# Optimization experiments

Hardware: AMD Instinct MI355X
Metric: run time of the kernel (lower is better)

Reference implementation:

```python
import jax, jax.numpy as jnp
import numpy as np

H = 64    # n_hidden
N = 1535  # input nodes; total graph nodes Nn = N + 1
B = 32    # batch
BN_EPS = 1e-5


def _p(key, shape, scale=0.05):
    return (jax.random.normal(key, shape, dtype=jnp.float32) * scale)


def setup_inputs() -> dict:
    key = jax.random.key(0)
    ks = jax.random.split(key, 32)
    inp = {
        'input_xx': jax.random.normal(ks[0], (B, N, 8), dtype=jnp.float32),
        'input_yy': jax.random.normal(ks[1], (B, N), dtype=jnp.float32),
        'output_xx': jax.random.normal(ks[2], (B, 1, 8), dtype=jnp.float32),
        # fc1: Linear(9, H); fc2: Linear(H, H)
        'W1': _p(ks[3], (H, 9)), 'b1': _p(ks[4], (H,)),
        'W2': _p(ks[5], (H, H)), 'b2': _p(ks[6], (H,)),
        # enc_new_x: Linear(8, H)
        'Wenc': _p(ks[7], (H, 8)), 'benc': _p(ks[8], (H,)),
        # Q, K, V: Linear(H, H)
        'WQ': _p(ks[9], (H, H)), 'bQ': _p(ks[10], (H,)),
        'WK': _p(ks[11], (H, H)), 'bK': _p(ks[12], (H,)),
        'WV': _p(ks[13], (H, H)), 'bV': _p(ks[14], (H,)),
        # QK: Linear(2H, 1) split into the q-half and k-half of its weight row
        'wQKq': _p(ks[15], (H,)), 'wQKk': _p(ks[16], (H,)),
        'bQK': _p(ks[17], ()),
        # A2N: Linear(H, H)
        'WA': _p(ks[18], (H, H)), 'bA': _p(ks[19], (H,)),
        # BatchNorm1d affine params
        'gamma': jnp.ones((H,), jnp.float32), 'beta': jnp.zeros((H,), jnp.float32),
        # heads
        'Wmu': _p(ks[20], (1, H)), 'bmu': _p(ks[21], (1,)),
        'Wsig': _p(ks[22], (1, H)), 'bsig': _p(ks[23], (1,)),
    }
    return inp


def _forward(input_xx, input_yy, output_xx, W1, b1, W2, b2, Wenc, benc,
             WQ, bQ, WK, bK, WV, bV, wQKq, wQKk, bQK, WA, bA,
             gamma, beta, Wmu, bmu, Wsig, bsig):
    # encode input nodes: cat(x, y) -> fc1 -> relu -> fc2 -> relu
    x = jnp.concatenate([input_xx, input_yy[..., None]], axis=-1)  # [B,N,9]
    h = jax.nn.relu(x @ W1.T + b1)
    h = jax.nn.relu(h @ W2.T + b2)                                  # [B,N,H]
    out_enc = jax.nn.relu(output_xx[:, 0, :] @ Wenc.T + benc)       # [B,H]
    # nodes: [Nn, B, H]  (node axis first, matching the torch list of nodes)
    nodes = jnp.concatenate([jnp.transpose(h, (1, 0, 2)), out_enc[None]], axis=0)

    def communicate(nodes):
        q = nodes @ WQ.T + bQ  # [Nn,B,H]
        k = nodes @ WK.T + bK
        v = nodes @ WV.T + bV
        # QK(cat(q,k)) decomposes additively: score[i,b,j] = q[i,b].wq + k[j,b].wk + b
        sq = q @ wQKq          # [Nn,B]
        sk = k @ wQKk          # [Nn,B]
        scores = sq[:, :, None] + sk.T[None, :, :] + bQK  # [Nn,B,Nn]
        w_att = jax.nn.softmax(scores, axis=-1)
        aggre = jnp.einsum('ibj,jbh->ibh', w_att, v)      # [Nn,B,H]
        z = aggre @ WA.T + bA
        # BatchNorm1d in training mode, applied per node over the batch axis
        mu = jnp.mean(z, axis=1, keepdims=True)
        var = jnp.var(z, axis=1, keepdims=True)
        z = (z - mu) / jnp.sqrt(var + BN_EPS) * gamma + beta
        return jax.nn.relu(z)

    for _ in range(4):
        nodes = communicate(nodes)

    agg = jnp.max(nodes, axis=0)                # [B,H]
    mu_out = agg @ Wmu.T + bmu                  # [B,1]
    sig_out = (agg @ Wsig.T + bsig) ** 2 + 0.01 # [B,1]
    return mu_out, sig_out


def reference(input_xx, input_yy, output_xx, W1, b1, W2, b2, Wenc, benc,
              WQ, bQ, WK, bK, WV, bV, wQKq, wQKk, bQK, WA, bA,
              gamma, beta, Wmu, bmu, Wsig, bsig):
    return _forward(input_xx, input_yy, output_xx, W1, b1, W2, b2, Wenc, benc,
                    WQ, bQ, WK, bK, WV, bV, wQKq, wQKk, bQK, WA, bA,
                    gamma, beta, Wmu, bmu, Wsig, bsig)
```

## Files before the change

kernel.cpp:

```cpp
#include <hip/hip_runtime.h>
#include <math.h>

#define HD    64
#define NIN   1535
#define NN    1536
#define BB    32
#define BN_EPS 1e-5f
#define CH    64
#define NCH   24

#define WS_M  0
#define WS_S  768
#define WS_V  1536

__global__ __launch_bounds__(256) void k_main(
    const float* __restrict__ xx,
    const float* __restrict__ yy,
    const float* __restrict__ oxx,
    const float* __restrict__ W1, const float* __restrict__ b1,
    const float* __restrict__ W2, const float* __restrict__ b2,
    const float* __restrict__ Wenc, const float* __restrict__ benc,
    const float* __restrict__ WK, const float* __restrict__ wQKk,
    float* __restrict__ ws) {
  __shared__ float W1s[576];
  __shared__ float b1s[64], b2s[64], bencs[64], us[64];
  __shared__ float Wencs[512];
  __shared__ float W2Ts[64 * 65];
  __shared__ float xs[512];
  __shared__ float ys[64];
  __shared__ float h1s[4][64];
  __shared__ float h2s[64 * 64];
  __shared__ float sks[64], e_s[64], rbuf[256], red0[1];

  const int t = threadIdx.x;
  const int blk = blockIdx.x;
  const int b = blk & 31;
  const int c = blk >> 5;
  const int pp = b * NCH + c;

  for (int e = t; e < 576; e += 256) W1s[e] = W1[e];
  for (int e = t; e < 512; e += 256) Wencs[e] = Wenc[e];
  for (int e = t; e < 4096; e += 256) {
    int h = e >> 6, k = e & 63;
    W2Ts[k * 65 + h] = W2[e];
  }
  for (int e = t; e < 512; e += 256) {
    int j = e >> 3, k = e & 7;
    int r0 = c * CH + j;
    xs[e] = (r0 < NIN) ? xx[(size_t)b * (NIN * 8) + (size_t)r0 * 8 + k]
                       : oxx[b * 8 + k];
  }
  if (t < 64) {
    b1s[t] = b1[t]; b2s[t] = b2[t]; bencs[t] = benc[t];
    int r0 = c * CH + t;
    ys[t] = (r0 < NIN) ? yy[b * NIN + r0] : 0.f;
    float a = 0.f;
    #pragma unroll
    for (int h0 = 0; h0 < 64; h0++) a += wQKk[h0] * WK[h0 * 64 + t];
    us[t] = a;
  }
  __syncthreads();

  const int w = t >> 6, lane = t & 63;
  float* h1w = h1s[w];

  float w2r[64];
  #pragma unroll
  for (int k = 0; k < 64; k++) w2r[k] = W2Ts[k * 65 + lane];

  for (int rr = 0; rr < 16; rr++) {
    int j = w * 16 + rr;
    int r0 = c * CH + j;
    const float* xr = xs + j * 8;
    float h2;
    if (r0 < NIN) {
      const float* wr = W1s + lane * 9;
      float a = b1s[lane];
      a += xr[0] * wr[0] + xr[1] * wr[1] + xr[2] * wr[2] + xr[3] * wr[3];
      a += xr[4] * wr[4] + xr[5] * wr[5] + xr[6] * wr[6] + xr[7] * wr[7];
      a += ys[j] * wr[8];
      h1w[lane] = fmaxf(a, 0.f);
      float a0 = b2s[lane], a1 = 0.f;
      #pragma unroll
      for (int k = 0; k < 64; k += 4) {
        float4 hv = *(const float4*)(h1w + k);
        a0 += hv.x * w2r[k]     + hv.z * w2r[k + 2];
        a1 += hv.y * w2r[k + 1] + hv.w * w2r[k + 3];
      }
      h2 = fmaxf(a0 + a1, 0.f);
    } else {
      const float* wr = Wencs + lane * 8;
      float a = bencs[lane];
      #pragma unroll
      for (int k = 0; k < 8; k++) a += xr[k] * wr[k];
      h2 = fmaxf(a, 0.f);
    }
    h2s[j * 64 + lane] = h2;
    float p = h2 * us[lane];
    p += __shfl_down(p, 32); p += __shfl_down(p, 16); p += __shfl_down(p, 8);
    p += __shfl_down(p, 4);  p += __shfl_down(p, 2);  p += __shfl_down(p, 1);
    if (lane == 0) sks[j] = p;
  }
  __syncthreads();

  if (t < 64) {
    float m = sks[t];
    m = fmaxf(m, __shfl_down(m, 32)); m = fmaxf(m, __shfl_down(m, 16));
    m = fmaxf(m, __shfl_down(m, 8));  m = fmaxf(m, __shfl_down(m, 4));
    m = fmaxf(m, __shfl_down(m, 2));  m = fmaxf(m, __shfl_down(m, 1));
    if (t == 0) red0[0] = m;
  }
  __syncthreads();
  float M = red0[0];
  if (t < 64) {
    float e = expf(sks[t] - M);
    e_s[t] = e;
    float s = e;
    s += __shfl_down(s, 32); s += __shfl_down(s, 16); s += __shfl_down(s, 8);
    s += __shfl_down(s, 4);  s += __shfl_down(s, 2);  s += __shfl_down(s, 1);
    if (t == 0) { ws[WS_M + pp] = M; ws[WS_S + pp] = s; }
  }
  __syncthreads();
  {
    float acc = 0.f;
    for (int j = w; j < 64; j += 4) acc += e_s[j] * h2s[j * 64 + lane];
    rbuf[t] = acc;
    __syncthreads();
    if (t < 64)
      ws[WS_V + pp * 64 + t] =
          rbuf[t] + rbuf[64 + t] + rbuf[128 + t] + rbuf[192 + t];
  }
}

__global__ __launch_bounds__(256) void k_tail(
    const float* __restrict__ ws,
    const float* __restrict__ WV, const float* __restrict__ bV,
    const float* __restrict__ WA, const float* __restrict__ bA,
    const float* __restrict__ gamma, const float* __restrict__ beta,
    const float* __restrict__ Wmu, const float* __restrict__ bmu,
    const float* __restrict__ Wsig, const float* __restrict__ bsig,
    float* __restrict__ out) {
  __shared__ float WAs[64 * 65];
  __shared__ float WVs[4096];
  __shared__ float WAVT[4096];
  __shared__ float bAVs[64];
  __shared__ float Ml[768], Sl[768], wexp[768];
  __shared__ float Mb[32], iSb[32];
  __shared__ float st[32 * 66];
  __shared__ float zs[32 * 66];
  __shared__ float scs[64], shs[64];
  const int t = threadIdx.x;

  for (int e = t; e < 4096; e += 256) {
    int h = e >> 6, m = e & 63;
    WAs[h * 65 + m] = WA[e];
    WVs[e] = WV[e];
  }
  for (int p = t; p < 768; p += 256) {
    Ml[p] = ws[WS_M + p];
    Sl[p] = ws[WS_S + p];
  }
  __syncthreads();

  if (t < 64) {
    float a = bA[t];
    #pragma unroll
    for (int k = 0; k < 64; k++) a += WAs[t * 65 + k] * bV[k];
    bAVs[t] = a;
  }
  {
    int kg = t >> 6, h = t & 63;
    float acc[16];
    #pragma unroll
    for (int kk = 0; kk < 16; kk++) acc[kk] = 0.f;
    for (int m = 0; m < 64; m++) {
      float wa = WAs[h * 65 + m];
      const float4* wv = (const float4*)(WVs + m * 64 + kg * 16);
      float4 w0 = wv[0], w1 = wv[1], w2 = wv[2], w3 = wv[3];
      acc[0]  += wa * w0.x; acc[1]  += wa * w0.y; acc[2]  += wa * w0.z; acc[3]  += wa * w0.w;
      acc[4]  += wa * w1.x; acc[5]  += wa * w1.y; acc[6]  += wa * w1.z; acc[7]  += wa * w1.w;
      acc[8]  += wa * w2.x; acc[9]  += wa * w2.y; acc[10] += wa * w2.z; acc[11] += wa * w2.w;
      acc[12] += wa * w3.x; acc[13] += wa * w3.y; acc[14] += wa * w3.z; acc[15] += wa * w3.w;
    }
    #pragma unroll
    for (int kk = 0; kk < 16; kk++) WAVT[(kg * 16 + kk) * 64 + h] = acc[kk];
  }
  if (t < 32) {
    float m = -1e30f;
    for (int cc = 0; cc < NCH; cc++) m = fmaxf(m, Ml[t * NCH + cc]);
    Mb[t] = m;
  }
  __syncthreads();
  for (int p = t; p < 768; p += 256) {
    int bb = p / NCH;
    wexp[p] = expf(Ml[p] - Mb[bb]);
  }
  __syncthreads();
  if (t < 32) {
    float s = 0.f;
    for (int cc = 0; cc < NCH; cc++) {
      int p = t * NCH + cc;
      s += Sl[p] * wexp[p];
    }
    iSb[t] = 1.0f / s;
  }
  __syncthreads();
  {
    int bb = t >> 3, hg = t & 7;
    float acc[8];
    #pragma unroll
    for (int jj = 0; jj < 8; jj++) acc[jj] = 0.f;
    for (int cc = 0; cc < NCH; cc++) {
      int p = bb * NCH + cc;
      float wgt = wexp[p];
      const float* vp = ws + WS_V + p * 64 + hg;
      #pragma unroll
      for (int jj = 0; jj < 8; jj++) acc[jj] += wgt * vp[jj * 8];
    }
    float is = iSb[bb];
    #pragma unroll
    for (int jj = 0; jj < 8; jj++) st[bb * 66 + hg + 8 * jj] = acc[jj] * is;
  }
  __syncthreads();

  for (int r = 0; r < 4; r++) {
    {
      int bb = t >> 3, hg = t & 7;
      float acc[8];
      #pragma unroll
      for (int jj = 0; jj < 8; jj++) acc[jj] = bAVs[hg + 8 * jj];
      for (int k = 0; k < 64; k++) {
        float v = st[bb * 66 + k];
        const float* wp = WAVT + k * 64 + hg;
        #pragma unroll
        for (int jj = 0; jj < 8; jj++) acc[jj] += v * wp[8 * jj];
      }
      #pragma unroll
      for (int jj = 0; jj < 8; jj++) zs[bb * 66 + hg + 8 * jj] = acc[jj];
    }
    __syncthreads();
    if (t < 64) {
      float s1 = 0.f;
      for (int bb2 = 0; bb2 < BB; bb2++) s1 += zs[bb2 * 66 + t];
      float mu = s1 * (1.0f / BB);
      float s2 = 0.f;
      for (int bb2 = 0; bb2 < BB; bb2++) {
        float d = zs[bb2 * 66 + t] - mu;
        s2 += d * d;
      }
      float inv = gamma[t] / sqrtf(s2 * (1.0f / BB) + BN_EPS);
      scs[t] = inv;
      shs[t] = beta[t] - mu * inv;
    }
    __syncthreads();
    for (int e = t; e < BB * 64; e += 256) {
      int bb2 = e >> 6, hh = e & 63;
      st[bb2 * 66 + hh] = fmaxf(zs[bb2 * 66 + hh] * scs[hh] + shs[hh], 0.f);
    }
    __syncthreads();
  }

  if (t < BB) {
    const float* nr = st + t * 66;
    float m = bmu[0], sg = bsig[0];
    #pragma unroll 8
    for (int h = 0; h < 64; h++) {
      float v = nr[h];
      m += v * Wmu[h];
      sg += v * Wsig[h];
    }
    out[t] = m;
    out[BB + t] = sg * sg + 0.01f;
  }
}

extern "C" void kernel_launch(void* const* d_in, const int* in_sizes, int n_in,
                              void* d_out, int out_size, void* d_ws, size_t ws_size,
                              hipStream_t stream) {
  const float* xx   = (const float*)d_in[0];
  const float* yy   = (const float*)d_in[1];
  const float* oxx  = (const float*)d_in[2];
  const float* W1   = (const float*)d_in[3];
  const float* b1   = (const float*)d_in[4];
  const float* W2   = (const float*)d_in[5];
  const float* b2   = (const float*)d_in[6];
  const float* Wenc = (const float*)d_in[7];
  const float* benc = (const float*)d_in[8];
  const float* WK   = (const float*)d_in[11];
  const float* WV   = (const float*)d_in[13];
  const float* bV   = (const float*)d_in[14];
  const float* wQKk = (const float*)d_in[16];
  const float* WA   = (const float*)d_in[18];
  const float* bA   = (const float*)d_in[19];
  const float* gamma= (const float*)d_in[20];
  const float* beta = (const float*)d_in[21];
  const float* Wmu  = (const float*)d_in[22];
  const float* bmu  = (const float*)d_in[23];
  const float* Wsig = (const float*)d_in[24];
  const float* bsig = (const float*)d_in[25];

  float* ws  = (float*)d_ws;
  float* out = (float*)d_out;

  k_main<<<BB * NCH, 256, 0, stream>>>(xx, yy, oxx, W1, b1, W2, b2, Wenc, benc,
                                       WK, wQKk, ws);
  k_tail<<<1, 256, 0, stream>>>(ws, WV, bV, WA, bA, gamma, beta,
                                Wmu, bmu, Wsig, bsig, out);
}
```

Baseline: 148.2 us.

## Fuse main and tail kernels via last-block-done atomic counter

Merges the per-chunk encoder kernel and the single-block tail kernel into one launch, where the last block to finish (found with an atomic counter plus thread fences) runs the cross-chunk softmax merge, the folded WA·WV projection, the four BatchNorm rounds and the heads. Shared memory is unioned into one buffer, and WV is read straight from global memory instead of being staged. This removes one kernel launch and the gap between launches. In exchange it adds a memset launch for the counter, and the serial tail now runs inside a 768-block grid after the last block arrives.

```diff
diff --git a/kernel.cpp b/kernel.cpp
--- a/kernel.cpp
+++ b/kernel.cpp
@@ -8,269 +8,297 @@
 #define BN_EPS 1e-5f
 #define CH    64
 #define NCH   24
-
-#define WS_M  0
-#define WS_S  768
-#define WS_V  1536
-
-__global__ __launch_bounds__(256) void k_main(
-    const float* __restrict__ xx,
-    const float* __restrict__ yy,
+#define NBLK  (BB * NCH)
+
+#define WS_M   0
+#define WS_S   768
+#define WS_V   1536
+#define WS_CNT 50688
+#define CNT_BYTE_OFF (WS_CNT * 4)
+
+#define SM_W1  0
+#define SM_B1  576
+#define SM_B2  640
+#define SM_BE  704
+#define SM_U   768
+#define SM_WE  832
+#define SM_W2T 1344
+#define SM_X   5504
+#define SM_Y   6016
+#define SM_H1  6080
+#define SM_H2  6336
+#define SM_SK  10432
+#define SM_E   10496
+#define SM_RB  10560
+#define SM_R0  10816
+#define ST_WAVT 0
+#define ST_BAV  4096
+#define ST_ML   4160
+#define ST_SL   4928
+#define ST_WX   5696
+#define ST_MB   6464
+#define ST_ISB  6496
+#define ST_WA   6528
+#define ST_ST   6528
+#define ST_ZS   8640
+#define ST_SC   10752
+#define ST_SH   10816
+#define SMEM_F  10880
+
+__global__ __launch_bounds__(256) void k_fused(
+    const float* __restrict__ xx, const float* __restrict__ yy,
     const float* __restrict__ oxx,
     const float* __restrict__ W1, const float* __restrict__ b1,
     const float* __restrict__ W2, const float* __restrict__ b2,
     const float* __restrict__ Wenc, const float* __restrict__ benc,
     const float* __restrict__ WK, const float* __restrict__ wQKk,
-    float* __restrict__ ws) {
-  __shared__ float W1s[576];
-  __shared__ float b1s[64], b2s[64], bencs[64], us[64];
-  __shared__ float Wencs[512];
-  __shared__ float W2Ts[64 * 65];
-  __shared__ float xs[512];
-  __shared__ float ys[64];
-  __shared__ float h1s[4][64];
-  __shared__ float h2s[64 * 64];
-  __shared__ float sks[64], e_s[64], rbuf[256], red0[1];
-
+    const float* __restrict__ WV, const float* __restrict__ bV,
+    const float* __restrict__ WA, const float* __restrict__ bA,
+    const float* __restrict__ gamma, const float* __restrict__ beta,
+    const float* __restrict__ Wmu, const float* __restrict__ bmu,
+    const float* __restrict__ Wsig, const float* __restrict__ bsig,
+    float* __restrict__ ws, unsigned int* __restrict__ cnt,
+    float* __restrict__ out) {
+  __shared__ float S[SMEM_F];
   const int t = threadIdx.x;
   const int blk = blockIdx.x;
   const int b = blk & 31;
   const int c = blk >> 5;
   const int pp = b * NCH + c;
 
-  for (int e = t; e < 576; e += 256) W1s[e] = W1[e];
-  for (int e = t; e < 512; e += 256) Wencs[e] = Wenc[e];
-  for (int e = t; e < 4096; e += 256) {
-    int h = e >> 6, k = e & 63;
-    W2Ts[k * 65 + h] = W2[e];
+  {
+    float* W1s = S + SM_W1;  float* b1s = S + SM_B1;  float* b2s = S + SM_B2;
+    float* bencs = S + SM_BE; float* us = S + SM_U;   float* Wencs = S + SM_WE;
+    float* W2Ts = S + SM_W2T; float* xs = S + SM_X;   float* ys = S + SM_Y;
+    float* h2s = S + SM_H2;   float* sks = S + SM_SK; float* e_s = S + SM_E;
+    float* rbuf = S + SM_RB;  float* red0 = S + SM_R0;
+
+    for (int e = t; e < 576; e += 256) W1s[e] = W1[e];
+    for (int e = t; e < 512; e += 256) Wencs[e] = Wenc[e];
+    for (int e = t; e < 4096; e += 256) {
+      int h = e >> 6, k = e & 63;
+      W2Ts[k * 65 + h] = W2[e];
+    }
+    for (int e = t; e < 512; e += 256) {
+      int j = e >> 3, k = e & 7;
+      int r0 = c * CH + j;
+      xs[e] = (r0 < NIN) ? xx[(size_t)b * (NIN * 8) + (size_t)r0 * 8 + k]
+                         : oxx[b * 8 + k];
+    }
+    if (t < 64) {
+      b1s[t] = b1[t]; b2s[t] = b2[t]; bencs[t] = benc[t];
+      int r0 = c * CH + t;
+      ys[t] = (r0 < NIN) ? yy[b * NIN + r0] : 0.f;
+      float a = 0.f;
+      #pragma unroll
+      for (int h0 = 0; h0 < 64; h0++) a += wQKk[h0] * WK[h0 * 64 + t];
+      us[t] = a;
+    }
+    __syncthreads();
+
+    const int w = t >> 6, lane = t & 63;
+    float* h1w = S + SM_H1 + w * 64;
+
+    float w2r[64];
+    #pragma unroll
+    for (int k = 0; k < 64; k++) w2r[k] = W2Ts[k * 65 + lane];
+
+    for (int rr = 0; rr < 16; rr++) {
+      int j = w * 16 + rr;
+      int r0 = c * CH + j;
+      const float* xr = xs + j * 8;
+      float h2;
+      if (r0 < NIN) {
+        const float* wr = W1s + lane * 9;
+        float a = b1s[lane];
+        a += xr[0] * wr[0] + xr[1] * wr[1] + xr[2] * wr[2] + xr[3] * wr[3];
+        a += xr[4] * wr[4] + xr[5] * wr[5] + xr[6] * wr[6] + xr[7] * wr[7];
+        a += ys[j] * wr[8];
+        h1w[lane] = fmaxf(a, 0.f);
+        float a0 = b2s[lane], a1 = 0.f;
+        #pragma unroll
+        for (int k = 0; k < 64; k += 4) {
+          float4 hv = *(const float4*)(h1w + k);
+          a0 += hv.x * w2r[k]     + hv.z * w2r[k + 2];
+          a1 += hv.y * w2r[k + 1] + hv.w * w2r[k + 3];
+        }
+        h2 = fmaxf(a0 + a1, 0.f);
+      } else {
+        const float* wr = Wencs + lane * 8;
+        float a = bencs[lane];
+        #pragma unroll
+        for (int k = 0; k < 8; k++) a += xr[k] * wr[k];
+        h2 = fmaxf(a, 0.f);
+      }
+      h2s[j * 64 + lane] = h2;
+      float p = h2 * us[lane];
+      p += __shfl_down(p, 32); p += __shfl_down(p, 16); p += __shfl_down(p, 8);
+      p += __shfl_down(p, 4);  p += __shfl_down(p, 2);  p += __shfl_down(p, 1);
+      if (lane == 0) sks[j] = p;
+    }
+    __syncthreads();
+
+    if (t < 64) {
+      float m = sks[t];
+      m = fmaxf(m, __shfl_down(m, 32)); m = fmaxf(m, __shfl_down(m, 16));
+      m = fmaxf(m, __shfl_down(m, 8));  m = fmaxf(m, __shfl_down(m, 4));
+      m = fmaxf(m, __shfl_down(m, 2));  m = fmaxf(m, __shfl_down(m, 1));
+      if (t == 0) red0[0] = m;
+    }
+    __syncthreads();
+    float M = red0[0];
+    if (t < 64) {
+      float e = expf(sks[t] - M);
+      e_s[t] = e;
+      float s = e;
+      s += __shfl_down(s, 32); s += __shfl_down(s, 16); s += __shfl_down(s, 8);
+      s += __shfl_down(s, 4);  s += __shfl_down(s, 2);  s += __shfl_down(s, 1);
+      if (t == 0) { ws[WS_M + pp] = M; ws[WS_S + pp] = s; }
+    }
+    __syncthreads();
+    {
+      float acc = 0.f;
+      for (int j = w; j < 64; j += 4) acc += e_s[j] * h2s[j * 64 + lane];
+      rbuf[t] = acc;
+      __syncthreads();
+      if (t < 64)
+        ws[WS_V + pp * 64 + t] =
+            rbuf[t] + rbuf[64 + t] + rbuf[128 + t] + rbuf[192 + t];
+    }
   }
-  for (int e = t; e < 512; e += 256) {
-    int j = e >> 3, k = e & 7;
-    int r0 = c * CH + j;
-    xs[e] = (r0 < NIN) ? xx[(size_t)b * (NIN * 8) + (size_t)r0 * 8 + k]
-                       : oxx[b * 8 + k];
-  }
-  if (t < 64) {
-    b1s[t] = b1[t]; b2s[t] = b2[t]; bencs[t] = benc[t];
-    int r0 = c * CH + t;
-    ys[t] = (r0 < NIN) ? yy[b * NIN + r0] : 0.f;
-    float a = 0.f;
-    #pragma unroll
-    for (int h0 = 0; h0 < 64; h0++) a += wQKk[h0] * WK[h0 * 64 + t];
-    us[t] = a;
-  }
+
+  __threadfence();
   __syncthreads();
-
-  const int w = t >> 6, lane = t & 63;
-  float* h1w = h1s[w];
-
-  float w2r[64];
-  #pragma unroll
-  for (int k = 0; k < 64; k++) w2r[k] = W2Ts[k * 65 + lane];
-
-  for (int rr = 0; rr < 16; rr++) {
-    int j = w * 16 + rr;
-    int r0 = c * CH + j;
-    const float* xr = xs + j * 8;
-    float h2;
-    if (r0 < NIN) {
-      const float* wr = W1s + lane * 9;
-      float a = b1s[lane];
-      a += xr[0] * wr[0] + xr[1] * wr[1] + xr[2] * wr[2] + xr[3] * wr[3];
-      a += xr[4] * wr[4] + xr[5] * wr[5] + xr[6] * wr[6] + xr[7] * wr[7];
-      a += ys[j] * wr[8];
-      h1w[lane] = fmaxf(a, 0.f);
-      float a0 = b2s[lane], a1 = 0.f;
-      #pragma unroll
-      for (int k = 0; k < 64; k += 4) {
-        float4 hv = *(const float4*)(h1w + k);
-        a0 += hv.x * w2r[k]     + hv.z * w2r[k + 2];
-        a1 += hv.y * w2r[k + 1] + hv.w * w2r[k + 3];
-      }
-      h2 = fmaxf(a0 + a1, 0.f);
-    } else {
-      const float* wr = Wencs + lane * 8;
-      float a = bencs[lane];
-      #pragma unroll
-      for (int k = 0; k < 8; k++) a += xr[k] * wr[k];
-      h2 = fmaxf(a, 0.f);
-    }
-    h2s[j * 64 + lane] = h2;
-    float p = h2 * us[lane];
-    p += __shfl_down(p, 32); p += __shfl_down(p, 16); p += __shfl_down(p, 8);
-    p += __shfl_down(p, 4);  p += __shfl_down(p, 2);  p += __shfl_down(p, 1);
-    if (lane == 0) sks[j] = p;
-  }
+  if (t == 0) S[SM_R0] = (float)(atomicAdd(cnt, 1u) == NBLK - 1 ? 1 : 0);
   __syncthreads();
-
-  if (t < 64) {
-    float m = sks[t];
-    m = fmaxf(m, __shfl_down(m, 32)); m = fmaxf(m, __shfl_down(m, 16));
-    m = fmaxf(m, __shfl_down(m, 8));  m = fmaxf(m, __shfl_down(m, 4));
-    m = fmaxf(m, __shfl_down(m, 2));  m = fmaxf(m, __shfl_down(m, 1));
-    if (t == 0) red0[0] = m;
-  }
+  if (S[SM_R0] == 0.f) return;
+  __threadfence();
   __syncthreads();
-  float M = red0[0];
-  if (t < 64) {
-    float e = expf(sks[t] - M);
-    e_s[t] = e;
-    float s = e;
-    s += __shfl_down(s, 32); s += __shfl_down(s, 16); s += __shfl_down(s, 8);
-    s += __shfl_down(s, 4);  s += __shfl_down(s, 2);  s += __shfl_down(s, 1);
-    if (t == 0) { ws[WS_M + pp] = M; ws[WS_S + pp] = s; }
-  }
-  __syncthreads();
+
   {
-    float acc = 0.f;
-    for (int j = w; j < 64; j += 4) acc += e_s[j] * h2s[j * 64 + lane];
-    rbuf[t] = acc;
-    __syncthreads();
-    if (t < 64)
-      ws[WS_V + pp * 64 + t] =
-          rbuf[t] + rbuf[64 + t] + rbuf[128 + t] + rbuf[192 + t];
-  }
-}
-
-__global__ __launch_bounds__(256) void k_tail(
-    const float* __restrict__ ws,
-    const float* __restrict__ WV, const float* __restrict__ bV,
-    const float* __restrict__ WA, const float* __restrict__ bA,
-    const float* __restrict__ gamma, const float* __restrict__ beta,
-    const float* __restrict__ Wmu, const float* __restrict__ bmu,
-    const float* __restrict__ Wsig, const float* __restrict__ bsig,
-    float* __restrict__ out) {
-  __shared__ float WAs[64 * 65];
-  __shared__ float WVs[4096];
-  __shared__ float WAVT[4096];
-  __shared__ float bAVs[64];
-  __shared__ float Ml[768], Sl[768], wexp[768];
-  __shared__ float Mb[32], iSb[32];
-  __shared__ float st[32 * 66];
-  __shared__ float zs[32 * 66];
-  __shared__ float scs[64], shs[64];
-  const int t = threadIdx.x;
-
-  for (int e = t; e < 4096; e += 256) {
-    int h = e >> 6, m = e & 63;
-    WAs[h * 65 + m] = WA[e];
-    WVs[e] = WV[e];
-  }
-  for (int p = t; p < 768; p += 256) {
-    Ml[p] = ws[WS_M + p];
-    Sl[p] = ws[WS_S + p];
-  }
-  __syncthreads();
-
-  if (t < 64) {
-    float a = bA[t];
-    #pragma unroll
-    for (int k = 0; k < 64; k++) a += WAs[t * 65 + k] * bV[k];
-    bAVs[t] = a;
-  }
-  {
-    int kg = t >> 6, h = t & 63;
-    float acc[16];
-    #pragma unroll
-    for (int kk = 0; kk < 16; kk++) acc[kk] = 0.f;
-    for (int m = 0; m < 64; m++) {
-      float wa = WAs[h * 65 + m];
-      const float4* wv = (const float4*)(WVs + m * 64 + kg * 16);
-      float4 w0 = wv[0], w1 = wv[1], w2 = wv[2], w3 = wv[3];
-      acc[0]  += wa * w0.x; acc[1]  += wa * w0.y; acc[2]  += wa * w0.z; acc[3]  += wa * w0.w;
-      acc[4]  += wa * w1.x; acc[5]  += wa * w1.y; acc[6]  += wa * w1.z; acc[7]  += wa * w1.w;
-      acc[8]  += wa * w2.x; acc[9]  += wa * w2.y; acc[10] += wa * w2.z; acc[11] += wa * w2.w;
-      acc[12] += wa * w3.x; acc[13] += wa * w3.y; acc[14] += wa * w3.z; acc[15] += wa * w3.w;
-    }
-    #pragma unroll
-    for (int kk = 0; kk < 16; kk++) WAVT[(kg * 16 + kk) * 64 + h] = acc[kk];
-  }
-  if (t < 32) {
-    float m = -1e30f;
-    for (int cc = 0; cc < NCH; cc++) m = fmaxf(m, Ml[t * NCH + cc]);
-    Mb[t] = m;
-  }
-  __syncthreads();
-  for (int p = t; p < 768; p += 256) {
-    int bb = p / NCH;
-    wexp[p] = expf(Ml[p] - Mb[bb]);
-  }
-  __syncthreads();
-  if (t < 32) {
-    float s = 0.f;
-    for (int cc = 0; cc < NCH; cc++) {
-      int p = t * NCH + cc;
-      s += Sl[p] * wexp[p];
-    }
-    iSb[t] = 1.0f / s;
-  }
-  __syncthreads();
-  {
-    int bb = t >> 3, hg = t & 7;
-    float acc[8];
-    #pragma unroll
-    for (int jj = 0; jj < 8; jj++) acc[jj] = 0.f;
-    for (int cc = 0; cc < NCH; cc++) {
-      int p = bb * NCH + cc;
-      float wgt = wexp[p];
-      const float* vp = ws + WS_V + p * 64 + hg;
-      #pragma unroll
-      for (int jj = 0; jj < 8; jj++) acc[jj] += wgt * vp[jj * 8];
-    }
-    float is = iSb[bb];
-    #pragma unroll
-    for (int jj = 0; jj < 8; jj++) st[bb * 66 + hg + 8 * jj] = acc[jj] * is;
-  }
-  __syncthreads();
-
-  for (int r = 0; r < 4; r++) {
+    float* WAVT = S + ST_WAVT; float* bAVs = S + ST_BAV;
+    float* Ml = S + ST_ML;  float* Sl = S + ST_SL;  float* wexp = S + ST_WX;
+    float* Mb = S + ST_MB;  float* iSb = S + ST_ISB;
+    float* WAs = S + ST_WA; float* st = S + ST_ST;  float* zs = S + ST_ZS;
+    float* scs = S + ST_SC; float* shs = S + ST_SH;
+
+    for (int e = t; e < 4096; e += 256) {
+      int h = e >> 6, m = e & 63;
+      WAs[h * 65 + m] = WA[e];
+    }
+    for (int p = t; p < 768; p += 256) {
+      Ml[p] = ws[WS_M + p];
+      Sl[p] = ws[WS_S + p];
+    }
+    __syncthreads();
+
+    if (t < 64) {
+      float a = bA[t];
+      #pragma unroll
+      for (int k = 0; k < 64; k++) a += WAs[t * 65 + k] * bV[k];
+      bAVs[t] = a;
+    }
+    if (t < 32) {
+      float m = -1e30f;
+      for (int cc = 0; cc < NCH; cc++) m = fmaxf(m, Ml[t * NCH + cc]);
+      Mb[t] = m;
+    }
+    {
+      int kg = t >> 6, h = t & 63;
+      float acc[16];
+      #pragma unroll
+      for (int kk = 0; kk < 16; kk++) acc[kk] = 0.f;
+      for (int m = 0; m < 64; m++) {
+        float wa = WAs[h * 65 + m];
+        const float4* wv = (const float4*)(WV + m * 64 + kg * 16);
+        float4 w0 = wv[0], w1 = wv[1], w2 = wv[2], w3 = wv[3];
+        acc[0]  += wa * w0.x; acc[1]  += wa * w0.y; acc[2]  += wa * w0.z; acc[3]  += wa * w0.w;
+        acc[4]  += wa * w1.x; acc[5]  += wa * w1.y; acc[6]  += wa * w1.z; acc[7]  += wa * w1.w;
+        acc[8]  += wa * w2.x; acc[9]  += wa * w2.y; acc[10] += wa * w2.z; acc[11] += wa * w2.w;
+        acc[12] += wa * w3.x; acc[13] += wa * w3.y; acc[14] += wa * w3.z; acc[15] += wa * w3.w;
+      }
+      #pragma unroll
+      for (int kk = 0; kk < 16; kk++) WAVT[(kg * 16 + kk) * 64 + h] = acc[kk];
+    }
+    __syncthreads();
+    for (int p = t; p < 768; p += 256) wexp[p] = expf(Ml[p] - Mb[p / NCH]);
+    __syncthreads();
+    if (t < 32) {
+      float s = 0.f;
+      for (int cc = 0; cc < NCH; cc++) {
+        int p = t * NCH + cc;
+        s += Sl[p] * wexp[p];
+      }
+      iSb[t] = 1.0f / s;
+    }
+    __syncthreads();
     {
       int bb = t >> 3, hg = t & 7;
       float acc[8];
       #pragma unroll
-      for (int jj = 0; jj < 8; jj++) acc[jj] = bAVs[hg + 8 * jj];
-      for (int k = 0; k < 64; k++) {
-        float v = st[bb * 66 + k];
-        const float* wp = WAVT + k * 64 + hg;
-        #pragma unroll
-        for (int jj = 0; jj < 8; jj++) acc[jj] += v * wp[8 * jj];
-      }
-      #pragma unroll
-      for (int jj = 0; jj < 8; jj++) zs[bb * 66 + hg + 8 * jj] = acc[jj];
-    }
-    __syncthreads();
-    if (t < 64) {
-      float s1 = 0.f;
-      for (int bb2 = 0; bb2 < BB; bb2++) s1 += zs[bb2 * 66 + t];
-      float mu = s1 * (1.0f / BB);
-      float s2 = 0.f;
-      for (int bb2 = 0; bb2 < BB; bb2++) {
-        float d = zs[bb2 * 66 + t] - mu;
-        s2 += d * d;
-      }
-      float inv = gamma[t] / sqrtf(s2 * (1.0f / BB) + BN_EPS);
-      scs[t] = inv;
-      shs[t] = beta[t] - mu * inv;
-    }
-    __syncthreads();
-    for (int e = t; e < BB * 64; e += 256) {
-      int bb2 = e >> 6, hh = e & 63;
-      st[bb2 * 66 + hh] = fmaxf(zs[bb2 * 66 + hh] * scs[hh] + shs[hh], 0.f);
-    }
-    __syncthreads();
-  }
-
-  if (t < BB) {
-    const float* nr = st + t * 66;
-    float m = bmu[0], sg = bsig[0];
-    #pragma unroll 8
-    for (int h = 0; h < 64; h++) {
-      float v = nr[h];
-      m += v * Wmu[h];
-      sg += v * Wsig[h];
-    }
-    out[t] = m;
-    out[BB + t] = sg * sg + 0.01f;
+      for (int jj = 0; jj < 8; jj++) acc[jj] = 0.f;
+      for (int cc = 0; cc < NCH; cc++) {
+        int p = bb * NCH + cc;
+        float wgt = wexp[p];
+        const float* vp = ws + WS_V + p * 64 + hg;
+        #pragma unroll
+        for (int jj = 0; jj < 8; jj++) acc[jj] += wgt * vp[jj * 8];
+      }
+      float is = iSb[bb];
+      #pragma unroll
+      for (int jj = 0; jj < 8; jj++) st[bb * 66 + hg + 8 * jj] = acc[jj] * is;
+    }
+    __syncthreads();
+
+    for (int r = 0; r < 4; r++) {
+      {
+        int bb = t >> 3, hg = t & 7;
+        float acc[8];
+        #pragma unroll
+        for (int jj = 0; jj < 8; jj++) acc[jj] = bAVs[hg + 8 * jj];
+        for (int k = 0; k < 64; k++) {
+          float v = st[bb * 66 + k];
+          const float* wp = WAVT + k * 64 + hg;
+          #pragma unroll
+          for (int jj = 0; jj < 8; jj++) acc[jj] += v * wp[8 * jj];
+        }
+        #pragma unroll
+        for (int jj = 0; jj < 8; jj++) zs[bb * 66 + hg + 8 * jj] = acc[jj];
+      }
+      __syncthreads();
+      if (t < 64) {
+        float s1 = 0.f;
+        for (int bb2 = 0; bb2 < BB; bb2++) s1 += zs[bb2 * 66 + t];
+        float mu = s1 * (1.0f / BB);
+        float s2 = 0.f;
+        for (int bb2 = 0; bb2 < BB; bb2++) {
+          float d = zs[bb2 * 66 + t] - mu;
+          s2 += d * d;
+        }
+        float inv = gamma[t] / sqrtf(s2 * (1.0f / BB) + BN_EPS);
+        scs[t] = inv;
+        shs[t] = beta[t] - mu * inv;
+      }
+      __syncthreads();
+      for (int e = t; e < BB * 64; e += 256) {
+        int bb2 = e >> 6, hh = e & 63;
+        st[bb2 * 66 + hh] = fmaxf(zs[bb2 * 66 + hh] * scs[hh] + shs[hh], 0.f);
+      }
+      __syncthreads();
+    }
+
+    if (t < BB) {
+      const float* nr = st + t * 66;
+      float m = bmu[0], sg = bsig[0];
+      #pragma unroll 8
+      for (int h = 0; h < 64; h++) {
+        float v = nr[h];
+        m += v * Wmu[h];
+        sg += v * Wsig[h];
+      }
+      out[t] = m;
+      out[BB + t] = sg * sg + 0.01f;
+    }
   }
 }
 
@@ -299,11 +327,12 @@
   const float* Wsig = (const float*)d_in[24];
   const float* bsig = (const float*)d_in[25];
 
-  float* ws  = (float*)d_ws;
+  float* ws = (float*)d_ws;
+  unsigned int* cnt = (unsigned int*)((char*)d_ws + CNT_BYTE_OFF);
   float* out = (float*)d_out;
 
-  k_main<<<BB * NCH, 256, 0, stream>>>(xx, yy, oxx, W1, b1, W2, b2, Wenc, benc,
-                                       WK, wQKk, ws);
-  k_tail<<<1, 256, 0, stream>>>(ws, WV, bV, WA, bA, gamma, beta,
-                                Wmu, bmu, Wsig, bsig, out);
+  hipMemsetAsync(cnt, 0, 4, stream);
+  k_fused<<<NBLK, 256, 0, stream>>>(xx, yy, oxx, W1, b1, W2, b2, Wenc, benc,
+                                    WK, wQKk, WV, bV, WA, bA, gamma, beta,
+                                    Wmu, bmu, Wsig, bsig, ws, cnt, out);
 }
```

Measured after the change: 206.9 us. 39.6% more time.

## Move WA·WV precompute into extra main-kernel block and use online softmax per wave

Applied to the files above, without the earlier changes.

Adds one extra block to the main grid that computes the WA·WV product and fused bias into workspace, so the single-block tail kernel no longer does that serial matmul. The main kernel drops the shared-memory weight staging and instead loads W1/W2 rows straight into registers. It broadcasts h1 across lanes with readlane rather than through LDS. An online softmax per wave replaces the stored h2 tile and its multi-pass reductions. This cuts shared memory and barriers, at the cost of more global weight reads per block and faster-but-less-precise __expf.

```diff
diff --git a/kernel.cpp b/kernel.cpp
--- a/kernel.cpp
+++ b/kernel.cpp
@@ -1,57 +1,79 @@
 #include <hip/hip_runtime.h>
 #include <math.h>
 
-#define HD    64
 #define NIN   1535
 #define NN    1536
 #define BB    32
 #define BN_EPS 1e-5f
 #define CH    64
 #define NCH   24
-
-#define WS_M  0
-#define WS_S  768
-#define WS_V  1536
+#define NBLK  (BB * NCH)
+
+#define WS_M    0
+#define WS_S    768
+#define WS_V    1536
+#define WS_WAVT 50688
+#define WS_BAV  54784
+
+__device__ __forceinline__ float rdlane(float v, int l) {
+  return __int_as_float(__builtin_amdgcn_readlane(__float_as_int(v), l));
+}
 
 __global__ __launch_bounds__(256) void k_main(
-    const float* __restrict__ xx,
-    const float* __restrict__ yy,
+    const float* __restrict__ xx, const float* __restrict__ yy,
     const float* __restrict__ oxx,
     const float* __restrict__ W1, const float* __restrict__ b1,
     const float* __restrict__ W2, const float* __restrict__ b2,
     const float* __restrict__ Wenc, const float* __restrict__ benc,
     const float* __restrict__ WK, const float* __restrict__ wQKk,
+    const float* __restrict__ WV, const float* __restrict__ bV,
+    const float* __restrict__ WA, const float* __restrict__ bA,
     float* __restrict__ ws) {
-  __shared__ float W1s[576];
-  __shared__ float b1s[64], b2s[64], bencs[64], us[64];
-  __shared__ float Wencs[512];
-  __shared__ float W2Ts[64 * 65];
   __shared__ float xs[512];
   __shared__ float ys[64];
-  __shared__ float h1s[4][64];
-  __shared__ float h2s[64 * 64];
-  __shared__ float sks[64], e_s[64], rbuf[256], red0[1];
+  __shared__ float us[64];
+  __shared__ float cm[4], cs[4];
+  __shared__ float cvec[4][64];
 
   const int t = threadIdx.x;
   const int blk = blockIdx.x;
+
+  if (blk == NBLK) {
+    int kg = t >> 6, h = t & 63;
+    float acc[16];
+    #pragma unroll
+    for (int kk = 0; kk < 16; kk++) acc[kk] = 0.f;
+    for (int m = 0; m < 64; m++) {
+      float wa = WA[h * 64 + m];
+      const float4* wv = (const float4*)(WV + m * 64 + kg * 16);
+      float4 w0 = wv[0], w1 = wv[1], w2 = wv[2], w3 = wv[3];
+      acc[0]  += wa * w0.x; acc[1]  += wa * w0.y; acc[2]  += wa * w0.z; acc[3]  += wa * w0.w;
+      acc[4]  += wa * w1.x; acc[5]  += wa * w1.y; acc[6]  += wa * w1.z; acc[7]  += wa * w1.w;
+      acc[8]  += wa * w2.x; acc[9]  += wa * w2.y; acc[10] += wa * w2.z; acc[11] += wa * w2.w;
+      acc[12] += wa * w3.x; acc[13] += wa * w3.y; acc[14] += wa * w3.z; acc[15] += wa * w3.w;
+    }
+    #pragma unroll
+    for (int kk = 0; kk < 16; kk++)
+      ws[WS_WAVT + (kg * 16 + kk) * 64 + h] = acc[kk];
+    if (t < 64) {
+      float a = bA[t];
+      #pragma unroll
+      for (int k = 0; k < 64; k++) a += WA[t * 64 + k] * bV[k];
+      ws[WS_BAV + t] = a;
+    }
+    return;
+  }
+
   const int b = blk & 31;
   const int c = blk >> 5;
   const int pp = b * NCH + c;
 
-  for (int e = t; e < 576; e += 256) W1s[e] = W1[e];
-  for (int e = t; e < 512; e += 256) Wencs[e] = Wenc[e];
-  for (int e = t; e < 4096; e += 256) {
-    int h = e >> 6, k = e & 63;
-    W2Ts[k * 65 + h] = W2[e];
-  }
   for (int e = t; e < 512; e += 256) {
     int j = e >> 3, k = e & 7;
     int r0 = c * CH + j;
-    xs[e] = (r0 < NIN) ? xx[(size_t)b * (NIN * 8) + (size_t)r0 * 8 + k]
-                       : oxx[b * 8 + k];
+    xs[e] = (r0 < NIN) ? xx[((size_t)b * NIN + r0) * 8 + k] : oxx[b * 8 + k];
   }
   if (t < 64) {
-    b1s[t] = b1[t]; b2s[t] = b2[t]; bencs[t] = benc[t];
     int r0 = c * CH + t;
     ys[t] = (r0 < NIN) ? yy[b * NIN + r0] : 0.f;
     float a = 0.f;
@@ -62,86 +84,85 @@
   __syncthreads();
 
   const int w = t >> 6, lane = t & 63;
-  float* h1w = h1s[w];
 
   float w2r[64];
+  {
+    const float4* wr = (const float4*)(W2 + lane * 64);
+    #pragma unroll
+    for (int q = 0; q < 16; q++) {
+      float4 v = wr[q];
+      w2r[4 * q] = v.x; w2r[4 * q + 1] = v.y;
+      w2r[4 * q + 2] = v.z; w2r[4 * q + 3] = v.w;
+    }
+  }
+  float w1r[9];
   #pragma unroll
-  for (int k = 0; k < 64; k++) w2r[k] = W2Ts[k * 65 + lane];
-
+  for (int i = 0; i < 9; i++) w1r[i] = W1[lane * 9 + i];
+  const float b1v = b1[lane], b2v = b2[lane], uv = us[lane];
+
+  float m_run = -1e30f, s_run = 0.f, acc_v = 0.f;
   for (int rr = 0; rr < 16; rr++) {
     int j = w * 16 + rr;
     int r0 = c * CH + j;
-    const float* xr = xs + j * 8;
+    float4 x0 = *(const float4*)(xs + j * 8);
+    float4 x1 = *(const float4*)(xs + j * 8 + 4);
     float h2;
     if (r0 < NIN) {
-      const float* wr = W1s + lane * 9;
-      float a = b1s[lane];
-      a += xr[0] * wr[0] + xr[1] * wr[1] + xr[2] * wr[2] + xr[3] * wr[3];
-      a += xr[4] * wr[4] + xr[5] * wr[5] + xr[6] * wr[6] + xr[7] * wr[7];
-      a += ys[j] * wr[8];
-      h1w[lane] = fmaxf(a, 0.f);
-      float a0 = b2s[lane], a1 = 0.f;
+      float a = b1v;
+      a += x0.x * w1r[0] + x0.y * w1r[1] + x0.z * w1r[2] + x0.w * w1r[3];
+      a += x1.x * w1r[4] + x1.y * w1r[5] + x1.z * w1r[6] + x1.w * w1r[7];
+      a += ys[j] * w1r[8];
+      float h1v = fmaxf(a, 0.f);
+      float a0 = b2v, a1 = 0.f, a2 = 0.f, a3 = 0.f;
       #pragma unroll
       for (int k = 0; k < 64; k += 4) {
-        float4 hv = *(const float4*)(h1w + k);
-        a0 += hv.x * w2r[k]     + hv.z * w2r[k + 2];
-        a1 += hv.y * w2r[k + 1] + hv.w * w2r[k + 3];
+        a0 += rdlane(h1v, k)     * w2r[k];
+        a1 += rdlane(h1v, k + 1) * w2r[k + 1];
+        a2 += rdlane(h1v, k + 2) * w2r[k + 2];
+        a3 += rdlane(h1v, k + 3) * w2r[k + 3];
       }
-      h2 = fmaxf(a0 + a1, 0.f);
+      h2 = fmaxf((a0 + a1) + (a2 + a3), 0.f);
     } else {
-      const float* wr = Wencs + lane * 8;
-      float a = bencs[lane];
-      #pragma unroll
-      for (int k = 0; k < 8; k++) a += xr[k] * wr[k];
+      const float4* we = (const float4*)(Wenc + lane * 8);
+      float4 w0 = we[0], w1v = we[1];
+      float a = benc[lane];
+      a += x0.x * w0.x + x0.y * w0.y + x0.z * w0.z + x0.w * w0.w;
+      a += x1.x * w1v.x + x1.y * w1v.y + x1.z * w1v.z + x1.w * w1v.w;
       h2 = fmaxf(a, 0.f);
     }
-    h2s[j * 64 + lane] = h2;
-    float p = h2 * us[lane];
-    p += __shfl_down(p, 32); p += __shfl_down(p, 16); p += __shfl_down(p, 8);
-    p += __shfl_down(p, 4);  p += __shfl_down(p, 2);  p += __shfl_down(p, 1);
-    if (lane == 0) sks[j] = p;
-  }
-  __syncthreads();
-
+    float p = h2 * uv;
+    p += __shfl_xor(p, 1);  p += __shfl_xor(p, 2);  p += __shfl_xor(p, 4);
+    p += __shfl_xor(p, 8);  p += __shfl_xor(p, 16); p += __shfl_xor(p, 32);
+    float mn = fmaxf(m_run, p);
+    float f  = __expf(m_run - mn);
+    float e  = __expf(p - mn);
+    s_run = s_run * f + e;
+    acc_v = acc_v * f + e * h2;
+    m_run = mn;
+  }
+
+  if (lane == 0) { cm[w] = m_run; cs[w] = s_run; }
+  cvec[w][lane] = acc_v;
+  __syncthreads();
   if (t < 64) {
-    float m = sks[t];
-    m = fmaxf(m, __shfl_down(m, 32)); m = fmaxf(m, __shfl_down(m, 16));
-    m = fmaxf(m, __shfl_down(m, 8));  m = fmaxf(m, __shfl_down(m, 4));
-    m = fmaxf(m, __shfl_down(m, 2));  m = fmaxf(m, __shfl_down(m, 1));
-    if (t == 0) red0[0] = m;
-  }
-  __syncthreads();
-  float M = red0[0];
-  if (t < 64) {
-    float e = expf(sks[t] - M);
-    e_s[t] = e;
-    float s = e;
-    s += __shfl_down(s, 32); s += __shfl_down(s, 16); s += __shfl_down(s, 8);
-    s += __shfl_down(s, 4);  s += __shfl_down(s, 2);  s += __shfl_down(s, 1);
-    if (t == 0) { ws[WS_M + pp] = M; ws[WS_S + pp] = s; }
-  }
-  __syncthreads();
-  {
-    float acc = 0.f;
-    for (int j = w; j < 64; j += 4) acc += e_s[j] * h2s[j * 64 + lane];
-    rbuf[t] = acc;
-    __syncthreads();
-    if (t < 64)
-      ws[WS_V + pp * 64 + t] =
-          rbuf[t] + rbuf[64 + t] + rbuf[128 + t] + rbuf[192 + t];
+    float M = fmaxf(fmaxf(cm[0], cm[1]), fmaxf(cm[2], cm[3]));
+    float f0 = __expf(cm[0] - M), f1 = __expf(cm[1] - M);
+    float f2 = __expf(cm[2] - M), f3 = __expf(cm[3] - M);
+    ws[WS_V + pp * 64 + t] = f0 * cvec[0][t] + f1 * cvec[1][t] +
+                             f2 * cvec[2][t] + f3 * cvec[3][t];
+    if (t == 0) {
+      ws[WS_M + pp] = M;
+      ws[WS_S + pp] = f0 * cs[0] + f1 * cs[1] + f2 * cs[2] + f3 * cs[3];
+    }
   }
 }
 
 __global__ __launch_bounds__(256) void k_tail(
     const float* __restrict__ ws,
-    const float* __restrict__ WV, const float* __restrict__ bV,
-    const float* __restrict__ WA, const float* __restrict__ bA,
     const float* __restrict__ gamma, const float* __restrict__ beta,
     const float* __restrict__ Wmu, const float* __restrict__ bmu,
     const float* __restrict__ Wsig, const float* __restrict__ bsig,
     float* __restrict__ out) {
-  __shared__ float WAs[64 * 65];
-  __shared__ float WVs[4096];
   __shared__ float WAVT[4096];
   __shared__ float bAVs[64];
   __shared__ float Ml[768], Sl[768], wexp[768];
@@ -151,50 +172,21 @@
   __shared__ float scs[64], shs[64];
   const int t = threadIdx.x;
 
-  for (int e = t; e < 4096; e += 256) {
-    int h = e >> 6, m = e & 63;
-    WAs[h * 65 + m] = WA[e];
-    WVs[e] = WV[e];
-  }
+  for (int e = t; e < 4096; e += 256) WAVT[e] = ws[WS_WAVT + e];
+  if (t < 64) bAVs[t] = ws[WS_BAV + t];
   for (int p = t; p < 768; p += 256) {
     Ml[p] = ws[WS_M + p];
     Sl[p] = ws[WS_S + p];
   }
   __syncthreads();
 
-  if (t < 64) {
-    float a = bA[t];
-    #pragma unroll
-    for (int k = 0; k < 64; k++) a += WAs[t * 65 + k] * bV[k];
-    bAVs[t] = a;
-  }
-  {
-    int kg = t >> 6, h = t & 63;
-    float acc[16];
-    #pragma unroll
-    for (int kk = 0; kk < 16; kk++) acc[kk] = 0.f;
-    for (int m = 0; m < 64; m++) {
-      float wa = WAs[h * 65 + m];
-      const float4* wv = (const float4*)(WVs + m * 64 + kg * 16);
-      float4 w0 = wv[0], w1 = wv[1], w2 = wv[2], w3 = wv[3];
-      acc[0]  += wa * w0.x; acc[1]  += wa * w0.y; acc[2]  += wa * w0.z; acc[3]  += wa * w0.w;
-      acc[4]  += wa * w1.x; acc[5]  += wa * w1.y; acc[6]  += wa * w1.z; acc[7]  += wa * w1.w;
-      acc[8]  += wa * w2.x; acc[9]  += wa * w2.y; acc[10] += wa * w2.z; acc[11] += wa * w2.w;
-      acc[12] += wa * w3.x; acc[13] += wa * w3.y; acc[14] += wa * w3.z; acc[15] += wa * w3.w;
-    }
-    #pragma unroll
-    for (int kk = 0; kk < 16; kk++) WAVT[(kg * 16 + kk) * 64 + h] = acc[kk];
-  }
   if (t < 32) {
     float m = -1e30f;
     for (int cc = 0; cc < NCH; cc++) m = fmaxf(m, Ml[t * NCH + cc]);
     Mb[t] = m;
   }
   __syncthreads();
-  for (int p = t; p < 768; p += 256) {
-    int bb = p / NCH;
-    wexp[p] = expf(Ml[p] - Mb[bb]);
-  }
+  for (int p = t; p < 768; p += 256) wexp[p] = __expf(Ml[p] - Mb[p / NCH]);
   __syncthreads();
   if (t < 32) {
     float s = 0.f;
@@ -302,8 +294,7 @@
   float* ws  = (float*)d_ws;
   float* out = (float*)d_out;
 
-  k_main<<<BB * NCH, 256, 0, stream>>>(xx, yy, oxx, W1, b1, W2, b2, Wenc, benc,
-                                       WK, wQKk, ws);
-  k_tail<<<1, 256, 0, stream>>>(ws, WV, bV, WA, bA, gamma, beta,
-                                Wmu, bmu, Wsig, bsig, out);
+  k_main<<<NBLK + 1, 256, 0, stream>>>(xx, yy, oxx, W1, b1, W2, b2, Wenc, benc,
+                                       WK, wQKk, WV, bV, WA, bA, ws);
+  k_tail<<<1, 256, 0, stream>>>(ws, gamma, beta, Wmu, bmu, Wsig, bsig, out);
 }
```

Result: no change. 148.9 us (+0.5%).
